# Kernel tuning notes

Hardware: AMD Instinct MI355X
Metric: run time of the kernel (lower is better)

Reference implementation:

```python
import jax, jax.numpy as jnp
import numpy as np
import math

D_MODEL = 1024
N_HEADS = 16
D_HID = 64
B, L = 2, 2048
NEG = -1e9
EPS = 1e-5


def setup_inputs() -> dict:
    key = jax.random.key(0)
    ks = jax.random.split(key, 16)
    dmh = N_HEADS * D_HID
    s_in = 1.0 / math.sqrt(D_MODEL)
    s_out = 1.0 / math.sqrt(dmh)
    return {
        "Q": jax.random.normal(ks[0], (B, L, D_MODEL), jnp.float32),
        "K": jax.random.normal(ks[1], (B, L, D_MODEL), jnp.float32),
        "V": jax.random.normal(ks[2], (B, L, D_MODEL), jnp.float32),
        "atten_mask": jax.random.randint(ks[3], (B, L, L), 0, 2) > 0,
        "Wq": jax.random.normal(ks[4], (D_MODEL, dmh), jnp.float32) * s_in,
        "bq": jnp.zeros((dmh,), jnp.float32),
        "Wk": jax.random.normal(ks[5], (D_MODEL, dmh), jnp.float32) * s_in,
        "bk": jnp.zeros((dmh,), jnp.float32),
        "Wv": jax.random.normal(ks[6], (D_MODEL, dmh), jnp.float32) * s_in,
        "bv": jnp.zeros((dmh,), jnp.float32),
        "Wo": jax.random.normal(ks[7], (dmh, D_MODEL), jnp.float32) * s_out,
        "bo": jnp.zeros((D_MODEL,), jnp.float32),
        "gamma": jnp.ones((D_MODEL,), jnp.float32),
        "beta": jnp.zeros((D_MODEL,), jnp.float32),
    }


def reference(Q, K, V, atten_mask, Wq, bq, Wk, bk, Wv, bv, Wo, bo, gamma, beta):
    b = Q.shape[0]
    # project and split heads: [B, L, H, Dh] -> [B, H, L, Dh]
    q = (Q @ Wq + bq).reshape(b, -1, N_HEADS, D_HID).transpose(0, 2, 1, 3)
    k = (K @ Wk + bk).reshape(b, -1, N_HEADS, D_HID).transpose(0, 2, 1, 3)
    v = (V @ Wv + bv).reshape(b, -1, N_HEADS, D_HID).transpose(0, 2, 1, 3)
    scale = 1.0 / math.sqrt(D_HID)
    scores = jnp.einsum("bhqd,bhkd->bhqk", q, k * scale)
    scores = jnp.where(atten_mask[:, None, :, :], NEG, scores)
    atten = jax.nn.softmax(scores, axis=-1)
    context = jnp.einsum("bhqk,bhkd->bhqd", atten, v)
    context = context.transpose(0, 2, 1, 3).reshape(b, -1, N_HEADS * D_HID)
    out = context @ Wo + bo
    # residual + LayerNorm
    x = out + Q
    mu = jnp.mean(x, axis=-1, keepdims=True)
    var = jnp.var(x, axis=-1, keepdims=True)
    y = (x - mu) * jax.lax.rsqrt(var + EPS) * gamma + beta
    return (y, atten)
```

## Files before the change

### kernel.cpp

```cpp
#include <hip/hip_runtime.h>
#include <hip/hip_fp16.h>

typedef unsigned short u16;
typedef __attribute__((ext_vector_type(8))) _Float16 f16x8;
typedef __attribute__((ext_vector_type(2))) _Float16 f16x2;
typedef __attribute__((ext_vector_type(4))) float   f32x4;

typedef const __attribute__((address_space(1))) void* gas1_t;
typedef __attribute__((address_space(3))) void*       las3_t;

#define LOG2E 1.44269504089f
#define M12   17.3123404907f

__device__ __forceinline__ void async_ld16(const void* g, void* s){
  __builtin_amdgcn_global_load_lds((gas1_t)g, (las3_t)s, 16, 0, 0);
}
__device__ __forceinline__ u16 f2h(float f){
  return __half_as_ushort(__float2half(f));
}

__global__ void cvt3_kernel(const float* __restrict__ s0, const float* __restrict__ s1,
                            const float* __restrict__ s2, u16* __restrict__ d0,
                            u16* __restrict__ d1, u16* __restrict__ d2)
{
  const float* s = (blockIdx.y==0)? s0 : (blockIdx.y==1)? s1 : s2;
  u16* d = (blockIdx.y==0)? d0 : (blockIdx.y==1)? d1 : d2;
  for(int i = blockIdx.x*256 + threadIdx.x; i < 1048576; i += 512*256){
    float4 v = ((const float4*)s)[i];
    ushort4 o; o.x=f2h(v.x); o.y=f2h(v.y); o.z=f2h(v.z); o.w=f2h(v.w);
    ((ushort4*)d)[i] = o;
  }
}

__global__ void transcvt_kernel(const float* __restrict__ W0, const float* __restrict__ W1,
                                const float* __restrict__ W2, const float* __restrict__ W3,
                                u16* __restrict__ T0, u16* __restrict__ T1,
                                u16* __restrict__ T2, u16* __restrict__ T3)
{
  __shared__ float tile[64][65];
  int z = blockIdx.z;
  const float* W = (z==0)?W0:(z==1)?W1:(z==2)?W2:W3;
  u16* T = (z==0)?T0:(z==1)?T1:(z==2)?T2:T3;
  int k0 = blockIdx.y*64, n0v = blockIdx.x*64;
  int t = threadIdx.x, r = t>>4, c4 = (t&15)*4;
#pragma unroll
  for(int p=0;p<4;p++){
    int rr = p*16 + r;
    float4 v = *(const float4*)&W[(size_t)(k0+rr)*1024 + n0v + c4];
    tile[rr][c4+0]=v.x; tile[rr][c4+1]=v.y; tile[rr][c4+2]=v.z; tile[rr][c4+3]=v.w;
  }
  __syncthreads();
#pragma unroll
  for(int p=0;p<4;p++){
    int rr = p*16 + r;
    ushort4 o;
    o.x = f2h(tile[c4+0][rr]); o.y = f2h(tile[c4+1][rr]);
    o.z = f2h(tile[c4+2][rr]); o.w = f2h(tile[c4+3][rr]);
    *(ushort4*)&T[(size_t)(n0v+rr)*1024 + k0 + c4] = o;
  }
}

__global__ void mask_detect_kernel(const unsigned int* __restrict__ m, int* __restrict__ flag){
  __shared__ int any;
  if(threadIdx.x==0) any = 0;
  __syncthreads();
  int bad = 0;
  for(int i=threadIdx.x;i<2048;i+=256) if(m[i] > 1u) bad = 1;
  if(bad) any = 1;
  __syncthreads();
  if(threadIdx.x==0) *flag = any;
}

__global__ void mask_bits_kernel(const void* __restrict__ msrc, const int* __restrict__ flag,
                                 unsigned long long* __restrict__ mbits)
{
  int gw = (blockIdx.x*256 + threadIdx.x)>>6;
  int lane = threadIdx.x & 63;
  int f = *flag;
  for(int c=0;c<32;c++){
    int idx = gw*2048 + c*64 + lane;
    unsigned v = f ? (unsigned)((const unsigned char*)msrc)[idx]
                   : ((const unsigned int*)msrc)[idx];
    unsigned long long bal = __ballot(v != 0u);
    if(lane==0) mbits[gw*32 + c] = bal;
  }
}

__device__ __forceinline__ void gemm_kloop(const u16* __restrict__ A, const u16* __restrict__ BT,
                                           int m0, int n0, u16* lA, u16* lB, f32x4 acc[4][4])
{
  int t = threadIdx.x, w = t>>6, l = t&63, l4 = l>>4, lm = l&15;
  int wr = w>>1, wc = w&1;
  for(int k0=0;k0<1024;k0+=32){
#pragma unroll
    for(int j=0;j<2;j++){
      int idx = j*4096 + w*1024 + l*16;
      int r = idx>>6, cb = idx&63;
      int cbs = cb ^ ((r&3)<<4);
      async_ld16((const char*)A  + (((size_t)(m0+r))<<11) + k0*2 + cbs,
                 (char*)lA + j*4096 + w*1024);
      async_ld16((const char*)BT + (((size_t)(n0+r))<<11) + k0*2 + cbs,
                 (char*)lB + j*4096 + w*1024);
    }
    __syncthreads();
    f16x8 af[4], bfr[4];
#pragma unroll
    for(int m=0;m<4;m++){
      int ar = wr*64 + m*16 + lm;
      af[m] = *(const f16x8*)((const char*)lA + ar*64 + ((l4*16) ^ ((ar&3)<<4)));
    }
#pragma unroll
    for(int n=0;n<4;n++){
      int br = wc*64 + n*16 + lm;
      bfr[n] = *(const f16x8*)((const char*)lB + br*64 + ((l4*16) ^ ((br&3)<<4)));
    }
#pragma unroll
    for(int m=0;m<4;m++)
#pragma unroll
      for(int n=0;n<4;n++)
        acc[m][n] = __builtin_amdgcn_mfma_f32_16x16x32_f16(af[m], bfr[n], acc[m][n], 0,0,0);
    __syncthreads();
  }
}

__global__ __launch_bounds__(256) void proj_gemm(
    const u16* __restrict__ Xq, const u16* __restrict__ Xk, const u16* __restrict__ Xv,
    const u16* __restrict__ WqT, const u16* __restrict__ WkT, const u16* __restrict__ WvT,
    const float* __restrict__ bq, const float* __restrict__ bk, const float* __restrict__ bv,
    u16* __restrict__ qb, u16* __restrict__ kbuf, u16* __restrict__ vTb)
{
  __shared__ u16 lA[4096], lB[4096];
  int z = blockIdx.z;
  const u16* A  = (z==0)?Xq :(z==1)?Xk :Xv;
  const u16* BT = (z==0)?WqT:(z==1)?WkT:WvT;
  const float* bias = (z==0)?bq:(z==1)?bk:bv;
  int m0 = blockIdx.y*128, n0 = blockIdx.x*128;
  f32x4 zf = {0.f,0.f,0.f,0.f};
  f32x4 acc[4][4];
#pragma unroll
  for(int m=0;m<4;m++)
#pragma unroll
    for(int n=0;n<4;n++) acc[m][n]=zf;
  gemm_kloop(A, BT, m0, n0, lA, lB, acc);

  int t = threadIdx.x, w = t>>6, l = t&63, l4 = l>>4, lm = l&15;
  int wr = w>>1, wc = w&1;
  float scale = (z==1)? 0.125f : 1.0f;
#pragma unroll
  for(int n=0;n<4;n++){
    int ng = n0 + wc*64 + n*16 + lm;
    float bsv = bias[ng];
#pragma unroll
    for(int m=0;m<4;m++){
      int mb = m0 + wr*64 + m*16 + l4*4;
      f32x4 c = acc[m][n];
      int bhh = ((mb>>11)<<4) + (ng>>6);
      if(z<2){
        u16* dst = (z==0)? qb : kbuf;
        size_t base = (((size_t)bhh)<<17) + ((size_t)(mb&2047)<<6) + (ng&63);
        dst[base      ] = f2h((c[0]+bsv)*scale);
        dst[base +  64] = f2h((c[1]+bsv)*scale);
        dst[base + 128] = f2h((c[2]+bsv)*scale);
        dst[base + 192] = f2h((c[3]+bsv)*scale);
      } else {
        size_t off = (((size_t)bhh)<<17) + ((size_t)(ng&63)<<11) + (mb&2047);
        ushort4 o;
        o.x=f2h(c[0]+bsv); o.y=f2h(c[1]+bsv); o.z=f2h(c[2]+bsv); o.w=f2h(c[3]+bsv);
        *(ushort4*)(vTb + off) = o;
      }
    }
  }
}

__global__ __launch_bounds__(256) void attn_fused(
    const u16* __restrict__ qb, const u16* __restrict__ kb,
    const u16* __restrict__ vTb, const unsigned long long* __restrict__ mbits,
    float* __restrict__ att, u16* __restrict__ ctx)
{
  __shared__ u16 ktile[4096];
  __shared__ u16 vtile[4096];
  __shared__ u16 pl[4][16*136];
  int fid = blockIdx.x;
  int xcd = fid & 7, pos = fid >> 3;
  int bh = (xcd<<2) + (pos>>5);
  int q0 = (pos & 31)*64;
  int b = bh>>4, h = bh&15;
  int t = threadIdx.x, w = t>>6, l = t&63, l4 = l>>4, lm = l&15;
  int qw = q0 + w*16 + lm;

  const u16* qrow = qb + ((size_t)bh*2048 + qw)*64;
  f16x8 qB0 = *(const f16x8*)(qrow + l4*8);
  f16x8 qB1 = *(const f16x8*)(qrow + 32 + l4*8);

  const unsigned long long* mrow = mbits + (size_t)(b*2048 + qw)*32;
  const char* kbase_b = (const char*)(kb  + ((size_t)bh<<17));
  const char* vbase_b = (const char*)(vTb + ((size_t)bh<<17));
  f32x4 zf = {0.f,0.f,0.f,0.f};

  float esum = 0.f;
  for(int kt=0;kt<32;kt++){
    int gk = kt*64;
#pragma unroll
    for(int j=0;j<2;j++){
      int idx = j*4096 + t*16, row = idx>>7, cb = idx&127;
      async_ld16(kbase_b + (size_t)(gk+row)*128 + (cb ^ ((row&7)<<4)),
                 (char*)ktile + idx);
    }
    __syncthreads();
    unsigned long long mw = mrow[kt];
    unsigned mlo = (unsigned)mw, mhi = (unsigned)(mw>>32);
#pragma unroll
    for(int kf=0;kf<4;kf++){
      int keyr = kf*16 + lm, sw = (keyr&7)<<4;
      const char* kp = (const char*)ktile + keyr*128;
      f16x8 a0 = *(const f16x8*)(kp + ((l4*16) ^ sw));
      f16x8 a1 = *(const f16x8*)(kp + ((64 + l4*16) ^ sw));
      f32x4 s = __builtin_amdgcn_mfma_f32_16x16x32_f16(a0, qB0, zf, 0,0,0);
      s = __builtin_amdgcn_mfma_f32_16x16x32_f16(a1, qB1, s, 0,0,0);
      unsigned nib = (((kf&2)?mhi:mlo) >> ((kf&1)*16 + l4*4)) & 15u;
      esum += exp2f(((nib&1u)? -1e9f : s[0])*LOG2E - M12);
      esum += exp2f(((nib&2u)? -1e9f : s[1])*LOG2E - M12);
      esum += exp2f(((nib&4u)? -1e9f : s[2])*LOG2E - M12);
      esum += exp2f(((nib&8u)? -1e9f : s[3])*LOG2E - M12);
    }
    __syncthreads();
  }
  esum += __shfl_xor(esum, 16);
  esum += __shfl_xor(esum, 32);
  float lrs = -M12 - log2f(fmaxf(esum, 1e-30f));

  f32x4 cacc[4] = {zf,zf,zf,zf};
  int q_hi = l>>5, koff = (l&31)*4;
  float* abase = att + ((size_t)bh*2048 + q0 + w*16)*2048;
  u16* plw = &pl[w][0];

  for(int kg=0; kg<16; kg++){
#pragma unroll
    for(int km=0; km<2; km++){
      int kt = kg*2 + km, gk = kt*64;
#pragma unroll
      for(int j=0;j<2;j++){
        int idx = j*4096 + t*16, row = idx>>7, cb = idx&127;
        async_ld16(kbase_b + (size_t)(gk+row)*128 + (cb ^ ((row&7)<<4)),
                   (char*)ktile + idx);
        async_ld16(vbase_b + (size_t)row*4096 + gk*2 + (cb ^ ((row&7)<<4)),
                   (char*)vtile + idx);
      }
      __syncthreads();
      unsigned long long mw = mrow[kt];
      unsigned mlo = (unsigned)mw, mhi = (unsigned)(mw>>32);
#pragma unroll
      for(int kf=0;kf<4;kf++){
        int keyr = kf*16 + lm, sw = (keyr&7)<<4;
        const char* kp = (const char*)ktile + keyr*128;
        f16x8 a0 = *(const f16x8*)(kp + ((l4*16) ^ sw));
        f16x8 a1 = *(const f16x8*)(kp + ((64 + l4*16) ^ sw));
        f32x4 s = __builtin_amdgcn_mfma_f32_16x16x32_f16(a0, qB0, zf, 0,0,0);
        s = __builtin_amdgcn_mfma_f32_16x16x32_f16(a1, qB1, s, 0,0,0);
        unsigned nib = (((kf&2)?mhi:mlo) >> ((kf&1)*16 + l4*4)) & 15u;
        float p0 = exp2f(((nib&1u)? -1e9f : s[0])*LOG2E + lrs);
        float p1 = exp2f(((nib&2u)? -1e9f : s[1])*LOG2E + lrs);
        float p2 = exp2f(((nib&4u)? -1e9f : s[2])*LOG2E + lrs);
        float p3 = exp2f(((nib&8u)? -1e9f : s[3])*LOG2E + lrs);
        uint2 pk;
        pk.x = __builtin_bit_cast(unsigned, __builtin_amdgcn_cvt_pkrtz(p0,p1));
        pk.y = __builtin_bit_cast(unsigned, __builtin_amdgcn_cvt_pkrtz(p2,p3));
        *(uint2*)(plw + lm*136 + km*64 + kf*16 + l4*4) = pk;
      }
#pragma unroll
      for(int kk=0;kk<2;kk++){
        f16x8 pb = *(const f16x8*)(plw + lm*136 + km*64 + kk*32 + l4*8);
#pragma unroll
        for(int mf=0;mf<4;mf++){
          int dr = mf*16 + lm;
          const char* vp = (const char*)vtile + dr*128;
          f16x8 av = *(const f16x8*)(vp + ((kk*64 + l4*16) ^ ((dr&7)<<4)));
          cacc[mf] = __builtin_amdgcn_mfma_f32_16x16x32_f16(av, pb, cacc[mf], 0,0,0);
        }
      }
      __syncthreads();
    }
#pragma unroll
    for(int qq=0; qq<16; qq+=2){
      int q = qq + q_hi;
      uint2 ph = *(const uint2*)(plw + q*136 + koff);
      f16x2 h0 = __builtin_bit_cast(f16x2, ph.x);
      f16x2 h1 = __builtin_bit_cast(f16x2, ph.y);
      f32x4 o4 = { (float)h0[0], (float)h0[1], (float)h1[0], (float)h1[1] };
      __builtin_nontemporal_store(o4,
          (f32x4*)(abase + (size_t)q*2048 + kg*128 + koff));
    }
  }
  int token = b*2048 + qw;
#pragma unroll
  for(int mf=0;mf<4;mf++){
    ushort4 o;
    o.x=f2h(cacc[mf][0]); o.y=f2h(cacc[mf][1]);
    o.z=f2h(cacc[mf][2]); o.w=f2h(cacc[mf][3]);
    *(ushort4*)(ctx + (size_t)token*1024 + h*64 + mf*16 + l4*4) = o;
  }
}

__global__ __launch_bounds__(256) void out_gemm(
    const u16* __restrict__ ctx, const u16* __restrict__ WoT,
    const float* __restrict__ bo, const float* __restrict__ Qres, float* __restrict__ xout)
{
  __shared__ u16 lA[4096], lB[4096];
  int m0 = blockIdx.y*128, n0 = blockIdx.x*128;
  f32x4 zf = {0.f,0.f,0.f,0.f};
  f32x4 acc[4][4];
#pragma unroll
  for(int m=0;m<4;m++)
#pragma unroll
    for(int n=0;n<4;n++) acc[m][n]=zf;
  gemm_kloop(ctx, WoT, m0, n0, lA, lB, acc);

  int t = threadIdx.x, w = t>>6, l = t&63, l4 = l>>4, lm = l&15;
  int wr = w>>1, wc = w&1;
#pragma unroll
  for(int n=0;n<4;n++){
    int ng = n0 + wc*64 + n*16 + lm;
    float bsv = bo[ng];
#pragma unroll
    for(int m=0;m<4;m++){
      int mb = m0 + wr*64 + m*16 + l4*4;
      f32x4 c = acc[m][n];
#pragma unroll
      for(int j=0;j<4;j++){
        size_t o = ((size_t)(mb+j)<<10) + ng;
        xout[o] = c[j] + bsv + Qres[o];
      }
    }
  }
}

__global__ void ln_kernel(const float* __restrict__ x, const float* __restrict__ gamma,
                          const float* __restrict__ beta, float* __restrict__ y)
{
  int row = blockIdx.x, t = threadIdx.x;
  float4 v = ((const float4*)(x + (size_t)row*1024))[t];
  float s  = v.x+v.y+v.z+v.w;
  float sq = v.x*v.x + v.y*v.y + v.z*v.z + v.w*v.w;
#pragma unroll
  for(int d=1; d<64; d<<=1){ s += __shfl_xor(s, d); sq += __shfl_xor(sq, d); }
  __shared__ float red[8];
  int w = t>>6, l = t&63;
  if(l==0){ red[w] = s; red[4+w] = sq; }
  __syncthreads();
  s  = red[0]+red[1]+red[2]+red[3];
  sq = red[4]+red[5]+red[6]+red[7];
  float mu  = s * 0.0009765625f;
  float var = sq * 0.0009765625f - mu*mu;
  float rs  = rsqrtf(var + 1e-5f);
  float4 g  = ((const float4*)gamma)[t];
  float4 be = ((const float4*)beta)[t];
  float4 o;
  o.x = (v.x-mu)*rs*g.x + be.x;
  o.y = (v.y-mu)*rs*g.y + be.y;
  o.z = (v.z-mu)*rs*g.z + be.z;
  o.w = (v.w-mu)*rs*g.w + be.w;
  ((float4*)(y + (size_t)row*1024))[t] = o;
}

extern "C" void kernel_launch(void* const* d_in, const int* in_sizes, int n_in,
                              void* d_out, int out_size, void* d_ws, size_t ws_size,
                              hipStream_t stream)
{
  (void)in_sizes; (void)n_in; (void)out_size; (void)ws_size;
  const float* Q    = (const float*)d_in[0];
  const float* K    = (const float*)d_in[1];
  const float* V    = (const float*)d_in[2];
  const void*  mraw = d_in[3];
  const float* Wq   = (const float*)d_in[4];
  const float* bq   = (const float*)d_in[5];
  const float* Wk   = (const float*)d_in[6];
  const float* bk   = (const float*)d_in[7];
  const float* Wv   = (const float*)d_in[8];
  const float* bv   = (const float*)d_in[9];
  const float* Wo   = (const float*)d_in[10];
  const float* bo   = (const float*)d_in[11];
  const float* gamma= (const float*)d_in[12];
  const float* beta = (const float*)d_in[13];

  char* ws = (char*)d_ws;
  const size_t MB = 1ull<<20;
  u16* WqT  = (u16*)(ws + 0*MB);
  u16* WkT  = (u16*)(ws + 2*MB);
  u16* WvT  = (u16*)(ws + 4*MB);
  u16* WoT  = (u16*)(ws + 6*MB);
  u16* Xq   = (u16*)(ws + 8*MB);
  u16* Xk   = (u16*)(ws + 16*MB);
  u16* Xv   = (u16*)(ws + 24*MB);
  u16* qb   = (u16*)(ws + 32*MB);
  u16* kbuf = (u16*)(ws + 40*MB);
  u16* vTb  = (u16*)(ws + 48*MB);
  u16* ctx  = (u16*)(ws + 56*MB);
  unsigned long long* mbits = (unsigned long long*)(ws + 8*MB);
  int* flag = (int*)(ws + 10*MB);
  float* xres = (float*)(ws + 16*MB);

  float* yout = (float*)d_out;
  float* att  = (float*)d_out + 4194304;

  cvt3_kernel<<<dim3(512,3,1), 256, 0, stream>>>(Q,K,V,Xq,Xk,Xv);
  transcvt_kernel<<<dim3(16,16,4), 256, 0, stream>>>(Wq,Wk,Wv,Wo,WqT,WkT,WvT,WoT);
  proj_gemm<<<dim3(8,32,3), 256, 0, stream>>>(Xq,Xk,Xv,WqT,WkT,WvT,bq,bk,bv,qb,kbuf,vTb);
  mask_detect_kernel<<<1,256,0,stream>>>((const unsigned int*)mraw, flag);
  mask_bits_kernel<<<1024,256,0,stream>>>(mraw, flag, mbits);
  attn_fused<<<1024, 256, 0, stream>>>(qb,kbuf,vTb,mbits,att,ctx);
  out_gemm<<<dim3(8,32), 256, 0, stream>>>(ctx,WoT,bo,Q,xres);
  ln_kernel<<<4096, 256, 0, stream>>>(xres,gamma,beta,yout);
}
```

Measured before the change: 268.5 us.

## Merge prep kernels, remap GEMM tiles per XCD, double attention K/V tile size

```diff
diff --git a/kernel.cpp b/kernel.cpp
--- a/kernel.cpp
+++ b/kernel.cpp
@@ -19,70 +19,76 @@
   return __half_as_ushort(__float2half(f));
 }
 
-__global__ void cvt3_kernel(const float* __restrict__ s0, const float* __restrict__ s1,
-                            const float* __restrict__ s2, u16* __restrict__ d0,
-                            u16* __restrict__ d1, u16* __restrict__ d2)
-{
-  const float* s = (blockIdx.y==0)? s0 : (blockIdx.y==1)? s1 : s2;
-  u16* d = (blockIdx.y==0)? d0 : (blockIdx.y==1)? d1 : d2;
-  for(int i = blockIdx.x*256 + threadIdx.x; i < 1048576; i += 512*256){
-    float4 v = ((const float4*)s)[i];
-    ushort4 o; o.x=f2h(v.x); o.y=f2h(v.y); o.z=f2h(v.z); o.w=f2h(v.w);
-    ((ushort4*)d)[i] = o;
-  }
-}
-
-__global__ void transcvt_kernel(const float* __restrict__ W0, const float* __restrict__ W1,
-                                const float* __restrict__ W2, const float* __restrict__ W3,
-                                u16* __restrict__ T0, u16* __restrict__ T1,
-                                u16* __restrict__ T2, u16* __restrict__ T3)
+__global__ void prep_kernel(const float* __restrict__ Q, const float* __restrict__ K,
+                            const float* __restrict__ V, const void* __restrict__ msrc,
+                            const float* __restrict__ Wq, const float* __restrict__ Wk,
+                            const float* __restrict__ Wv, const float* __restrict__ Wo,
+                            u16* __restrict__ Xq, u16* __restrict__ Xk, u16* __restrict__ Xv,
+                            unsigned long long* __restrict__ mbits,
+                            u16* __restrict__ WqT, u16* __restrict__ WkT,
+                            u16* __restrict__ WvT, u16* __restrict__ WoT)
 {
   __shared__ float tile[64][65];
-  int z = blockIdx.z;
-  const float* W = (z==0)?W0:(z==1)?W1:(z==2)?W2:W3;
-  u16* T = (z==0)?T0:(z==1)?T1:(z==2)?T2:T3;
-  int k0 = blockIdx.y*64, n0v = blockIdx.x*64;
-  int t = threadIdx.x, r = t>>4, c4 = (t&15)*4;
-#pragma unroll
-  for(int p=0;p<4;p++){
-    int rr = p*16 + r;
-    float4 v = *(const float4*)&W[(size_t)(k0+rr)*1024 + n0v + c4];
-    tile[rr][c4+0]=v.x; tile[rr][c4+1]=v.y; tile[rr][c4+2]=v.z; tile[rr][c4+3]=v.w;
-  }
-  __syncthreads();
-#pragma unroll
-  for(int p=0;p<4;p++){
-    int rr = p*16 + r;
-    ushort4 o;
-    o.x = f2h(tile[c4+0][rr]); o.y = f2h(tile[c4+1][rr]);
-    o.z = f2h(tile[c4+2][rr]); o.w = f2h(tile[c4+3][rr]);
-    *(ushort4*)&T[(size_t)(n0v+rr)*1024 + k0 + c4] = o;
-  }
-}
-
-__global__ void mask_detect_kernel(const unsigned int* __restrict__ m, int* __restrict__ flag){
-  __shared__ int any;
-  if(threadIdx.x==0) any = 0;
-  __syncthreads();
-  int bad = 0;
-  for(int i=threadIdx.x;i<2048;i+=256) if(m[i] > 1u) bad = 1;
-  if(bad) any = 1;
-  __syncthreads();
-  if(threadIdx.x==0) *flag = any;
-}
-
-__global__ void mask_bits_kernel(const void* __restrict__ msrc, const int* __restrict__ flag,
-                                 unsigned long long* __restrict__ mbits)
-{
-  int gw = (blockIdx.x*256 + threadIdx.x)>>6;
-  int lane = threadIdx.x & 63;
-  int f = *flag;
-  for(int c=0;c<32;c++){
-    int idx = gw*2048 + c*64 + lane;
-    unsigned v = f ? (unsigned)((const unsigned char*)msrc)[idx]
-                   : ((const unsigned int*)msrc)[idx];
-    unsigned long long bal = __ballot(v != 0u);
-    if(lane==0) mbits[gw*32 + c] = bal;
+  int bid = blockIdx.x, t = threadIdx.x;
+
+  if(bid < 1536){
+    int zy = bid >> 9, bx = bid & 511;
+    const float* s = (zy==0)? Q : (zy==1)? K : V;
+    u16* d = (zy==0)? Xq : (zy==1)? Xk : Xv;
+    for(int i = bx*256 + t; i < 1048576; i += 512*256){
+      float4 v = ((const float4*)s)[i];
+      ushort4 o; o.x=f2h(v.x); o.y=f2h(v.y); o.z=f2h(v.z); o.w=f2h(v.w);
+      ((ushort4*)d)[i] = o;
+    }
+    return;
+  }
+  if(bid < 2560){
+    __shared__ int any;
+    if(t==0) any = 0;
+    __syncthreads();
+    {
+      const unsigned int* m32 = (const unsigned int*)msrc;
+      int bad = 0;
+#pragma unroll
+      for(int i=0;i<8;i++) if(m32[t*8+i] > 1u) bad = 1;
+      if(bad) any = 1;
+    }
+    __syncthreads();
+    int f = any;
+    int mb = bid - 1536;
+    int gw = (mb*256 + t)>>6;
+    int lane = t & 63;
+    for(int c=0;c<32;c++){
+      int idx = gw*2048 + c*64 + lane;
+      unsigned v = f ? (unsigned)((const unsigned char*)msrc)[idx]
+                     : ((const unsigned int*)msrc)[idx];
+      unsigned long long bal = __ballot(v != 0u);
+      if(lane==0) mbits[gw*32 + c] = bal;
+    }
+    return;
+  }
+  {
+    int wb = bid - 2560;
+    int z = wb >> 8, rem = wb & 255;
+    const float* W = (z==0)?Wq:(z==1)?Wk:(z==2)?Wv:Wo;
+    u16* T = (z==0)?WqT:(z==1)?WkT:(z==2)?WvT:WoT;
+    int k0 = (rem>>4)*64, n0v = (rem&15)*64;
+    int r = t>>4, c4 = (t&15)*4;
+#pragma unroll
+    for(int p=0;p<4;p++){
+      int rr = p*16 + r;
+      float4 v = *(const float4*)&W[(size_t)(k0+rr)*1024 + n0v + c4];
+      tile[rr][c4+0]=v.x; tile[rr][c4+1]=v.y; tile[rr][c4+2]=v.z; tile[rr][c4+3]=v.w;
+    }
+    __syncthreads();
+#pragma unroll
+    for(int p=0;p<4;p++){
+      int rr = p*16 + r;
+      ushort4 o;
+      o.x = f2h(tile[c4+0][rr]); o.y = f2h(tile[c4+1][rr]);
+      o.z = f2h(tile[c4+2][rr]); o.w = f2h(tile[c4+3][rr]);
+      *(ushort4*)&T[(size_t)(n0v+rr)*1024 + k0 + c4] = o;
+    }
   }
 }
 
@@ -123,6 +129,12 @@
   }
 }
 
+__device__ __forceinline__ void gemm_tile_remap(int fid, int& m0, int& n0){
+  int wg = (fid & 7)*32 + (fid >> 3);
+  n0 = (wg & 7)*128;
+  m0 = (wg >> 3)*128;
+}
+
 __global__ __launch_bounds__(256) void proj_gemm(
     const u16* __restrict__ Xq, const u16* __restrict__ Xk, const u16* __restrict__ Xv,
     const u16* __restrict__ WqT, const u16* __restrict__ WkT, const u16* __restrict__ WvT,
@@ -130,11 +142,12 @@
     u16* __restrict__ qb, u16* __restrict__ kbuf, u16* __restrict__ vTb)
 {
   __shared__ u16 lA[4096], lB[4096];
-  int z = blockIdx.z;
+  int z = blockIdx.y;
   const u16* A  = (z==0)?Xq :(z==1)?Xk :Xv;
   const u16* BT = (z==0)?WqT:(z==1)?WkT:WvT;
   const float* bias = (z==0)?bq:(z==1)?bk:bv;
-  int m0 = blockIdx.y*128, n0 = blockIdx.x*128;
+  int m0, n0;
+  gemm_tile_remap(blockIdx.x, m0, n0);
   f32x4 zf = {0.f,0.f,0.f,0.f};
   f32x4 acc[4][4];
 #pragma unroll
@@ -172,13 +185,13 @@
   }
 }
 
-__global__ __launch_bounds__(256) void attn_fused(
+__global__ __launch_bounds__(256, 3) void attn_fused(
     const u16* __restrict__ qb, const u16* __restrict__ kb,
     const u16* __restrict__ vTb, const unsigned long long* __restrict__ mbits,
     float* __restrict__ att, u16* __restrict__ ctx)
 {
-  __shared__ u16 ktile[4096];
-  __shared__ u16 vtile[4096];
+  __shared__ u16 ktile[8192];
+  __shared__ u16 vtile[8192];
   __shared__ u16 pl[4][16*136];
   int fid = blockIdx.x;
   int xcd = fid & 7, pos = fid >> 3;
@@ -198,30 +211,34 @@
   f32x4 zf = {0.f,0.f,0.f,0.f};
 
   float esum = 0.f;
-  for(int kt=0;kt<32;kt++){
-    int gk = kt*64;
-#pragma unroll
-    for(int j=0;j<2;j++){
+  for(int kg=0;kg<16;kg++){
+    int gk = kg*128;
+#pragma unroll
+    for(int j=0;j<4;j++){
       int idx = j*4096 + t*16, row = idx>>7, cb = idx&127;
       async_ld16(kbase_b + (size_t)(gk+row)*128 + (cb ^ ((row&7)<<4)),
                  (char*)ktile + idx);
     }
     __syncthreads();
-    unsigned long long mw = mrow[kt];
-    unsigned mlo = (unsigned)mw, mhi = (unsigned)(mw>>32);
-#pragma unroll
-    for(int kf=0;kf<4;kf++){
-      int keyr = kf*16 + lm, sw = (keyr&7)<<4;
-      const char* kp = (const char*)ktile + keyr*128;
-      f16x8 a0 = *(const f16x8*)(kp + ((l4*16) ^ sw));
-      f16x8 a1 = *(const f16x8*)(kp + ((64 + l4*16) ^ sw));
-      f32x4 s = __builtin_amdgcn_mfma_f32_16x16x32_f16(a0, qB0, zf, 0,0,0);
-      s = __builtin_amdgcn_mfma_f32_16x16x32_f16(a1, qB1, s, 0,0,0);
-      unsigned nib = (((kf&2)?mhi:mlo) >> ((kf&1)*16 + l4*4)) & 15u;
-      esum += exp2f(((nib&1u)? -1e9f : s[0])*LOG2E - M12);
-      esum += exp2f(((nib&2u)? -1e9f : s[1])*LOG2E - M12);
-      esum += exp2f(((nib&4u)? -1e9f : s[2])*LOG2E - M12);
-      esum += exp2f(((nib&8u)? -1e9f : s[3])*LOG2E - M12);
+#pragma unroll
+    for(int km=0;km<2;km++){
+      int kt = kg*2 + km;
+      unsigned long long mw = mrow[kt];
+      unsigned mlo = (unsigned)mw, mhi = (unsigned)(mw>>32);
+#pragma unroll
+      for(int kf=0;kf<4;kf++){
+        int keyr = km*64 + kf*16 + lm, sw = (keyr&7)<<4;
+        const char* kp = (const char*)ktile + keyr*128;
+        f16x8 a0 = *(const f16x8*)(kp + ((l4*16) ^ sw));
+        f16x8 a1 = *(const f16x8*)(kp + ((64 + l4*16) ^ sw));
+        f32x4 s = __builtin_amdgcn_mfma_f32_16x16x32_f16(a0, qB0, zf, 0,0,0);
+        s = __builtin_amdgcn_mfma_f32_16x16x32_f16(a1, qB1, s, 0,0,0);
+        unsigned nib = (((kf&2)?mhi:mlo) >> ((kf&1)*16 + l4*4)) & 15u;
+        esum += exp2f(((nib&1u)? -1e9f : s[0])*LOG2E - M12);
+        esum += exp2f(((nib&2u)? -1e9f : s[1])*LOG2E - M12);
+        esum += exp2f(((nib&4u)? -1e9f : s[2])*LOG2E - M12);
+        esum += exp2f(((nib&8u)? -1e9f : s[3])*LOG2E - M12);
+      }
     }
     __syncthreads();
   }
@@ -235,23 +252,26 @@
   u16* plw = &pl[w][0];
 
   for(int kg=0; kg<16; kg++){
+    int gk = kg*128;
+#pragma unroll
+    for(int j=0;j<4;j++){
+      int idx = j*4096 + t*16;
+      int krow = idx>>7, kcb = idx&127;
+      async_ld16(kbase_b + (size_t)(gk+krow)*128 + (kcb ^ ((krow&7)<<4)),
+                 (char*)ktile + idx);
+      int vrow = idx>>8, vcb = idx&255;
+      async_ld16(vbase_b + (size_t)vrow*4096 + gk*2 + (vcb ^ ((vrow&7)<<4)),
+                 (char*)vtile + idx);
+    }
+    __syncthreads();
 #pragma unroll
     for(int km=0; km<2; km++){
-      int kt = kg*2 + km, gk = kt*64;
-#pragma unroll
-      for(int j=0;j<2;j++){
-        int idx = j*4096 + t*16, row = idx>>7, cb = idx&127;
-        async_ld16(kbase_b + (size_t)(gk+row)*128 + (cb ^ ((row&7)<<4)),
-                   (char*)ktile + idx);
-        async_ld16(vbase_b + (size_t)row*4096 + gk*2 + (cb ^ ((row&7)<<4)),
-                   (char*)vtile + idx);
-      }
-      __syncthreads();
+      int kt = kg*2 + km;
       unsigned long long mw = mrow[kt];
       unsigned mlo = (unsigned)mw, mhi = (unsigned)(mw>>32);
 #pragma unroll
       for(int kf=0;kf<4;kf++){
-        int keyr = kf*16 + lm, sw = (keyr&7)<<4;
+        int keyr = km*64 + kf*16 + lm, sw = (keyr&7)<<4;
         const char* kp = (const char*)ktile + keyr*128;
         f16x8 a0 = *(const f16x8*)(kp + ((l4*16) ^ sw));
         f16x8 a1 = *(const f16x8*)(kp + ((64 + l4*16) ^ sw));
@@ -273,12 +293,11 @@
 #pragma unroll
         for(int mf=0;mf<4;mf++){
           int dr = mf*16 + lm;
-          const char* vp = (const char*)vtile + dr*128;
-          f16x8 av = *(const f16x8*)(vp + ((kk*64 + l4*16) ^ ((dr&7)<<4)));
+          const char* vp = (const char*)vtile + dr*256;
+          f16x8 av = *(const f16x8*)(vp + ((km*128 + kk*64 + l4*16) ^ ((dr&7)<<4)));
           cacc[mf] = __builtin_amdgcn_mfma_f32_16x16x32_f16(av, pb, cacc[mf], 0,0,0);
         }
       }
-      __syncthreads();
     }
 #pragma unroll
     for(int qq=0; qq<16; qq+=2){
@@ -290,6 +309,7 @@
       __builtin_nontemporal_store(o4,
           (f32x4*)(abase + (size_t)q*2048 + kg*128 + koff));
     }
+    __syncthreads();
   }
   int token = b*2048 + qw;
 #pragma unroll
@@ -306,7 +326,8 @@
     const float* __restrict__ bo, const float* __restrict__ Qres, float* __restrict__ xout)
 {
   __shared__ u16 lA[4096], lB[4096];
-  int m0 = blockIdx.y*128, n0 = blockIdx.x*128;
+  int m0, n0;
+  gemm_tile_remap(blockIdx.x, m0, n0);
   f32x4 zf = {0.f,0.f,0.f,0.f};
   f32x4 acc[4][4];
 #pragma unroll
@@ -395,19 +416,16 @@
   u16* kbuf = (u16*)(ws + 40*MB);
   u16* vTb  = (u16*)(ws + 48*MB);
   u16* ctx  = (u16*)(ws + 56*MB);
-  unsigned long long* mbits = (unsigned long long*)(ws + 8*MB);
-  int* flag = (int*)(ws + 10*MB);
   float* xres = (float*)(ws + 16*MB);
 
   float* yout = (float*)d_out;
   float* att  = (float*)d_out + 4194304;
-
-  cvt3_kernel<<<dim3(512,3,1), 256, 0, stream>>>(Q,K,V,Xq,Xk,Xv);
-  transcvt_kernel<<<dim3(16,16,4), 256, 0, stream>>>(Wq,Wk,Wv,Wo,WqT,WkT,WvT,WoT);
-  proj_gemm<<<dim3(8,32,3), 256, 0, stream>>>(Xq,Xk,Xv,WqT,WkT,WvT,bq,bk,bv,qb,kbuf,vTb);
-  mask_detect_kernel<<<1,256,0,stream>>>((const unsigned int*)mraw, flag);
-  mask_bits_kernel<<<1024,256,0,stream>>>(mraw, flag, mbits);
+  unsigned long long* mbits = (unsigned long long*)d_out;
+
+  prep_kernel<<<3584, 256, 0, stream>>>(Q,K,V,mraw,Wq,Wk,Wv,Wo,
+                                        Xq,Xk,Xv,mbits,WqT,WkT,WvT,WoT);
+  proj_gemm<<<dim3(256,3), 256, 0, stream>>>(Xq,Xk,Xv,WqT,WkT,WvT,bq,bk,bv,qb,kbuf,vTb);
   attn_fused<<<1024, 256, 0, stream>>>(qb,kbuf,vTb,mbits,att,ctx);
-  out_gemm<<<dim3(8,32), 256, 0, stream>>>(ctx,WoT,bo,Q,xres);
+  out_gemm<<<256, 256, 0, stream>>>(ctx,WoT,bo,Q,xres);
   ln_kernel<<<4096, 256, 0, stream>>>(xres,gamma,beta,yout);
 }
```

Result: faster. 258.1 us (-3.9%).
